# Kernel optimization log

Measured on AMD Instinct MI355X. Metric: run time of the kernel, lower is better.

Reference implementation:

```python
import jax, jax.numpy as jnp
import numpy as np

N_LAYERS = 2
ALPHA = 0.3
HAS_NORM = True
N_USERS = 100000
N_ITEMS = 50000
NNZ = 6400000
D = 64


def setup_inputs() -> dict:
    key = jax.random.key(0)
    ks = jax.random.split(key, 11)
    N = N_USERS + N_ITEMS
    return {
        "image_feats": jax.random.normal(ks[0], (N_ITEMS, 4096), dtype=jnp.float32),
        "text_feats": jax.random.normal(ks[1], (N_ITEMS, 384), dtype=jnp.float32),
        "image_pref": jax.random.normal(ks[2], (N_USERS, D), dtype=jnp.float32),
        "text_pref": jax.random.normal(ks[3], (N_USERS, D), dtype=jnp.float32),
        "W_img": jax.random.normal(ks[4], (4096, D), dtype=jnp.float32) * 0.02,
        "b_img": jax.random.normal(ks[5], (D,), dtype=jnp.float32) * 0.02,
        "W_txt": jax.random.normal(ks[6], (384, D), dtype=jnp.float32) * 0.02,
        "b_txt": jax.random.normal(ks[7], (D,), dtype=jnp.float32) * 0.02,
        "adj_vals": jax.random.uniform(ks[8], (NNZ,), dtype=jnp.float32),
        "adj_rows": jax.random.randint(ks[9], (NNZ,), 0, N, dtype=jnp.int32),
        "adj_cols": jax.random.randint(ks[10], (NNZ,), 0, N, dtype=jnp.int32),
    }


def _l2norm(x):
    # F.normalize(x, dim=1): x / max(||x||_2, eps)
    n = jnp.sqrt(jnp.sum(x * x, axis=1, keepdims=True))
    return x / jnp.maximum(n, 1e-12)


def reference(image_feats, text_feats, image_pref, text_pref,
              W_img, b_img, W_txt, b_txt, adj_vals, adj_rows, adj_cols):
    n_users = image_pref.shape[0]
    n_items = image_feats.shape[0]
    N = n_users + n_items

    image_emb = image_feats @ W_img + b_img  # [n_items, D]
    text_emb = text_feats @ W_txt + b_txt    # [n_items, D]
    if HAS_NORM:
        image_emb = _l2norm(image_emb)
        text_emb = _l2norm(text_emb)

    ego_i = jnp.concatenate([image_pref, image_emb], axis=0)  # [N, D]
    ego_t = jnp.concatenate([text_pref, text_emb], axis=0)    # [N, D]

    def spmm(x):
        # sparse COO matmul: out[r] += v * x[c]
        return jax.ops.segment_sum(adj_vals[:, None] * x[adj_cols], adj_rows,
                                   num_segments=N)

    for _ in range(N_LAYERS):
        ego_i = spmm(ego_i) + ALPHA * ego_i
        ego_t = spmm(ego_t) + ALPHA * ego_t

    user_pref = jnp.concatenate([ego_i[:n_users], ego_t[:n_users]], axis=1)
    items = jnp.concatenate([ego_i[n_users:], ego_t[n_users:]], axis=1)
    return user_pref, items
```

## Files before the change

### kernel.cpp

```cpp
#include <hip/hip_runtime.h>

#define N_USERS 100000
#define N_ITEMS 50000
#define NTOT    150000
#define DD      64
#define NNZV    6400000
#define ALPHA_  0.3f

#define BSHIFT  9
#define NBUCK   293
#define CH      16384
#define NCH     391

static constexpr size_t SZ = (size_t)NTOT * DD;

typedef unsigned int   u32;
typedef unsigned short u16;
typedef __attribute__((ext_vector_type(8))) short bf16x8;
typedef __attribute__((ext_vector_type(4))) float f32x4;

__device__ __forceinline__ u16 f2bf(float f) {
    u32 u = __float_as_uint(f);
    u += 0x7fffu + ((u >> 16) & 1u);
    return (u16)(u >> 16);
}
__device__ __forceinline__ float bf_lo(u32 w) { return __uint_as_float(w << 16); }
__device__ __forceinline__ float bf_hi(u32 w) { return __uint_as_float(w & 0xffff0000u); }

__global__ __launch_bounds__(256) void convert_wf(const float* __restrict__ W,
                                                  u32* __restrict__ Wf, int K)
{
    int tid = blockIdx.x * 256 + threadIdx.x;
    int total = (K >> 5) * 1024;
    if (tid >= total) return;
    int d  = tid & 3;
    int l  = (tid >> 2) & 63;
    int nt = (tid >> 8) & 3;
    int ks = tid >> 10;
    int k   = (ks << 5) + ((l >> 4) << 3) + (d << 1);
    int col = (nt << 4) + (l & 15);
    u16 lo = f2bf(W[(size_t)k * DD + col]);
    u16 hi = f2bf(W[(size_t)(k + 1) * DD + col]);
    Wf[tid] = (u32)lo | ((u32)hi << 16);
}

__global__ __launch_bounds__(256) void gemm_mfma(
    const float* __restrict__ A, const int4* __restrict__ Wf4,
    const float* __restrict__ bias, u16* __restrict__ bfp, int M, int K)
{
    const int w  = threadIdx.x >> 6;
    const int l  = threadIdx.x & 63;
    const int lr = l & 15;
    const int lk = l >> 4;
    const int rbase = blockIdx.x * 64 + w * 16;

    f32x4 acc0 = {0.f,0.f,0.f,0.f}, acc1 = acc0, acc2 = acc0, acc3 = acc0;

    int gr = rbase + lr; if (gr >= M) gr = M - 1;
    const float* ap = A + (size_t)gr * K + lk * 8;

    for (int ks = 0; ks < K; ks += 32) {
        float4 a0 = *(const float4*)(ap + ks);
        float4 a1 = *(const float4*)(ap + ks + 4);
        int4 av;
        av.x = (int)((u32)f2bf(a0.x) | ((u32)f2bf(a0.y) << 16));
        av.y = (int)((u32)f2bf(a0.z) | ((u32)f2bf(a0.w) << 16));
        av.z = (int)((u32)f2bf(a1.x) | ((u32)f2bf(a1.y) << 16));
        av.w = (int)((u32)f2bf(a1.z) | ((u32)f2bf(a1.w) << 16));
        bf16x8 af = *(bf16x8*)&av;
        const int4* wp = Wf4 + (size_t)(ks >> 5) * 256 + l;
        int4 w0 = wp[0], w1 = wp[64], w2 = wp[128], w3 = wp[192];
        acc0 = __builtin_amdgcn_mfma_f32_16x16x32_bf16(af, *(bf16x8*)&w0, acc0, 0, 0, 0);
        acc1 = __builtin_amdgcn_mfma_f32_16x16x32_bf16(af, *(bf16x8*)&w1, acc1, 0, 0, 0);
        acc2 = __builtin_amdgcn_mfma_f32_16x16x32_bf16(af, *(bf16x8*)&w2, acc2, 0, 0, 0);
        acc3 = __builtin_amdgcn_mfma_f32_16x16x32_bf16(af, *(bf16x8*)&w3, acc3, 0, 0, 0);
    }

    float bv0 = bias[lr], bv1 = bias[16 + lr], bv2 = bias[32 + lr], bv3 = bias[48 + lr];
    #pragma unroll
    for (int r = 0; r < 4; ++r) {
        float v0 = acc0[r] + bv0;
        float v1 = acc1[r] + bv1;
        float v2 = acc2[r] + bv2;
        float v3 = acc3[r] + bv3;
        float s = v0*v0 + v1*v1 + v2*v2 + v3*v3;
        s += __shfl_xor(s, 1); s += __shfl_xor(s, 2);
        s += __shfl_xor(s, 4); s += __shfl_xor(s, 8);
        float inv = 1.f / fmaxf(sqrtf(s), 1e-12f);
        int row = rbase + lk * 4 + r;
        if (row < M) {
            u16* bp = bfp + (size_t)row * 128;
            bp[lr]      = f2bf(v0 * inv);
            bp[16 + lr] = f2bf(v1 * inv);
            bp[32 + lr] = f2bf(v2 * inv);
            bp[48 + lr] = f2bf(v3 * inv);
        }
    }
}

__global__ __launch_bounds__(256) void build_user(const float4* __restrict__ ip,
                                                  const float4* __restrict__ tp,
                                                  ushort4* __restrict__ Xbf)
{
    int i = blockIdx.x * 256 + threadIdx.x;
    if (i >= N_USERS * 16) return;
    int row = i >> 4, q = i & 15;
    float4 vi = ip[i];
    float4 vt = tp[i];
    ushort4 bi; bi.x = f2bf(vi.x); bi.y = f2bf(vi.y); bi.z = f2bf(vi.z); bi.w = f2bf(vi.w);
    ushort4 bt; bt.x = f2bf(vt.x); bt.y = f2bf(vt.y); bt.z = f2bf(vt.z); bt.w = f2bf(vt.w);
    Xbf[(size_t)row * 32 + q]      = bi;
    Xbf[(size_t)row * 32 + 16 + q] = bt;
}

__global__ __launch_bounds__(256) void bucket_cnt(const int* __restrict__ rows,
                                                  int* __restrict__ gbhist)
{
    __shared__ int cnt[NBUCK];
    int t = threadIdx.x;
    for (int i = t; i < NBUCK; i += 256) cnt[i] = 0;
    __syncthreads();
    int beg = blockIdx.x * CH;
    int end = beg + CH; if (end > NNZV) end = NNZV;
    for (int i = beg + t; i < end; i += 256)
        atomicAdd(&cnt[rows[i] >> BSHIFT], 1);
    __syncthreads();
    for (int i = t; i < NBUCK; i += 256)
        if (cnt[i]) atomicAdd(&gbhist[i], cnt[i]);
}

__global__ __launch_bounds__(512) void scan_nbuck(const int* __restrict__ gbhist,
                                                  int* __restrict__ gbstart,
                                                  int* __restrict__ gbcur)
{
    __shared__ int sh[512];
    int t = threadIdx.x;
    int v = (t < NBUCK) ? gbhist[t] : 0;
    sh[t] = v;
    __syncthreads();
    for (int off = 1; off < 512; off <<= 1) {
        int x = (t >= off) ? sh[t - off] : 0;
        __syncthreads();
        sh[t] += x;
        __syncthreads();
    }
    if (t < NBUCK) {
        int e = sh[t] - v;
        gbstart[t] = e;
        gbcur[t]   = e;
    }
}

__global__ __launch_bounds__(256) void sort_pass1(
    const float* __restrict__ vals, const int* __restrict__ rows,
    const int* __restrict__ cols, int* __restrict__ gbcur,
    int2* __restrict__ ptmp)
{
    __shared__ int cnt[NBUCK];
    __shared__ int base[NBUCK];
    int t = threadIdx.x;
    int beg = blockIdx.x * CH;
    int end = beg + CH; if (end > NNZV) end = NNZV;

    for (int i = t; i < NBUCK; i += 256) cnt[i] = 0;
    __syncthreads();
    for (int i = beg + t; i < end; i += 256)
        atomicAdd(&cnt[rows[i] >> BSHIFT], 1);
    __syncthreads();
    for (int i = t; i < NBUCK; i += 256) {
        int c = cnt[i];
        base[i] = c ? atomicAdd(&gbcur[i], c) : 0;
    }
    __syncthreads();
    for (int i = t; i < NBUCK; i += 256) cnt[i] = 0;
    __syncthreads();
    for (int i = beg + t; i < end; i += 256) {
        int r = rows[i];
        int b = r >> BSHIFT;
        int rank = atomicAdd(&cnt[b], 1);
        int p = base[b] + rank;
        ptmp[p] = make_int2(__float_as_int(vals[i]), cols[i] | ((r & 511) << 18));
    }
}

__global__ __launch_bounds__(256) void sort_pass2(
    const int2* __restrict__ ptmp, const int* __restrict__ gbstart,
    int2* __restrict__ spair, int* __restrict__ rstart)
{
    __shared__ int rcnt[512];
    __shared__ int cur[512];
    __shared__ int s2[256];
    const int b = blockIdx.x;
    const int t = threadIdx.x;
    const int bstart = gbstart[b];
    const int bend   = (b == NBUCK - 1) ? NNZV : gbstart[b + 1];

    rcnt[t] = 0; rcnt[t + 256] = 0;
    __syncthreads();
    for (int i = bstart + t; i < bend; i += 256)
        atomicAdd(&rcnt[(ptmp[i].y >> 18) & 511], 1);
    __syncthreads();

    int a0 = rcnt[2 * t], a1 = rcnt[2 * t + 1];
    s2[t] = a0 + a1;
    __syncthreads();
    for (int off = 1; off < 256; off <<= 1) {
        int x = (t >= off) ? s2[t - off] : 0;
        __syncthreads();
        s2[t] += x;
        __syncthreads();
    }
    int epair = s2[t] - (a0 + a1);
    int c0 = bstart + epair;
    int c1 = c0 + a0;
    cur[2 * t]     = c0;
    cur[2 * t + 1] = c1;
    int r0 = (b << BSHIFT) + 2 * t;
    if (r0 < NTOT)     rstart[r0]     = c0;
    if (r0 + 1 < NTOT) rstart[r0 + 1] = c1;
    __syncthreads();

    for (int i = bstart + t; i < bend; i += 256) {
        int2 v = ptmp[i];
        int p = atomicAdd(&cur[(v.y >> 18) & 511], 1);
        spair[p] = make_int2(v.x, v.y & 0x3FFFF);
    }
}

__global__ void set_tail(int* __restrict__ rstart)
{
    if (threadIdx.x == 0 && blockIdx.x == 0) rstart[NTOT] = NNZV;
}

__global__ __launch_bounds__(256) void spmm_wave(
    const int2* __restrict__ spair, const int* __restrict__ rstart,
    const u32* __restrict__ Xbf, float* __restrict__ Xout,
    u32* __restrict__ XbfOut)
{
    int row = blockIdx.x * 4 + (threadIdx.x >> 6);
    int t   = threadIdx.x & 63;
    int beg = rstart[row];
    int end = rstart[row + 1];
    float a0 = 0.f, a1 = 0.f, b0 = 0.f, b1 = 0.f;
    int j = beg;
    for (; j + 8 <= end; j += 8) {
        int2 p0 = spair[j];     int2 p1 = spair[j + 1];
        int2 p2 = spair[j + 2]; int2 p3 = spair[j + 3];
        int2 p4 = spair[j + 4]; int2 p5 = spair[j + 5];
        int2 p6 = spair[j + 6]; int2 p7 = spair[j + 7];
        u32 w0 = Xbf[(size_t)p0.y * 64 + t];
        u32 w1 = Xbf[(size_t)p1.y * 64 + t];
        u32 w2 = Xbf[(size_t)p2.y * 64 + t];
        u32 w3 = Xbf[(size_t)p3.y * 64 + t];
        u32 w4 = Xbf[(size_t)p4.y * 64 + t];
        u32 w5 = Xbf[(size_t)p5.y * 64 + t];
        u32 w6 = Xbf[(size_t)p6.y * 64 + t];
        u32 w7 = Xbf[(size_t)p7.y * 64 + t];
        float v0 = __int_as_float(p0.x), v1 = __int_as_float(p1.x);
        float v2 = __int_as_float(p2.x), v3 = __int_as_float(p3.x);
        float v4 = __int_as_float(p4.x), v5 = __int_as_float(p5.x);
        float v6 = __int_as_float(p6.x), v7 = __int_as_float(p7.x);
        a0 += v0 * bf_lo(w0); a1 += v0 * bf_hi(w0);
        b0 += v1 * bf_lo(w1); b1 += v1 * bf_hi(w1);
        a0 += v2 * bf_lo(w2); a1 += v2 * bf_hi(w2);
        b0 += v3 * bf_lo(w3); b1 += v3 * bf_hi(w3);
        a0 += v4 * bf_lo(w4); a1 += v4 * bf_hi(w4);
        b0 += v5 * bf_lo(w5); b1 += v5 * bf_hi(w5);
        a0 += v6 * bf_lo(w6); a1 += v6 * bf_hi(w6);
        b0 += v7 * bf_lo(w7); b1 += v7 * bf_hi(w7);
    }
    for (; j < end; ++j) {
        int2 p = spair[j];
        u32 w = Xbf[(size_t)p.y * 64 + t];
        float v = __int_as_float(p.x);
        a0 += v * bf_lo(w); a1 += v * bf_hi(w);
    }
    u32 xr = Xbf[(size_t)row * 64 + t];
    float o0 = a0 + b0 + ALPHA_ * bf_lo(xr);
    float o1 = a1 + b1 + ALPHA_ * bf_hi(xr);
    if (Xout)
        *(float2*)(Xout + (size_t)row * 128 + 2 * t) = make_float2(o0, o1);
    if (XbfOut)
        XbfOut[(size_t)row * 64 + t] = (u32)f2bf(o0) | ((u32)f2bf(o1) << 16);
}

__global__ __launch_bounds__(256) void copy4(const float4* __restrict__ src,
                                             float4* __restrict__ dst, int n4)
{
    int i = blockIdx.x * 256 + threadIdx.x;
    if (i < n4) dst[i] = src[i];
}

__global__ __launch_bounds__(256) void gemm_bias(
    const float* __restrict__ A, const float* __restrict__ W,
    const float* __restrict__ bias, float* __restrict__ C, int M, int K, int ldc)
{
    __shared__ float As2[16][64];
    __shared__ float Bs2[16][64];
    const int t  = threadIdx.x;
    const int tx = t & 15, ty = t >> 4;
    const int lr = t >> 2;
    const int lk = (t & 3) << 2;
    const int brow = t >> 4;
    const int bc   = (t & 15) << 2;
    const int block_row = blockIdx.x << 6;

    float acc[4][4] = {{0.f,0.f,0.f,0.f},{0.f,0.f,0.f,0.f},{0.f,0.f,0.f,0.f},{0.f,0.f,0.f,0.f}};
    const int grow = block_row + lr;
    const bool arow_ok = (grow < M);
    const float* Aptr = A + (size_t)grow * K;

    for (int k0 = 0; k0 < K; k0 += 16) {
        float4 av = make_float4(0.f, 0.f, 0.f, 0.f);
        if (arow_ok) av = *(const float4*)(Aptr + k0 + lk);
        As2[lk+0][lr] = av.x; As2[lk+1][lr] = av.y; As2[lk+2][lr] = av.z; As2[lk+3][lr] = av.w;
        *(float4*)&Bs2[brow][bc] = *(const float4*)(W + (size_t)(k0 + brow) * DD + bc);
        __syncthreads();
        #pragma unroll
        for (int k = 0; k < 16; ++k) {
            float4 a = *(const float4*)&As2[k][ty << 2];
            float4 b = *(const float4*)&Bs2[k][tx << 2];
            acc[0][0] += a.x*b.x; acc[0][1] += a.x*b.y; acc[0][2] += a.x*b.z; acc[0][3] += a.x*b.w;
            acc[1][0] += a.y*b.x; acc[1][1] += a.y*b.y; acc[1][2] += a.y*b.z; acc[1][3] += a.y*b.w;
            acc[2][0] += a.z*b.x; acc[2][1] += a.z*b.y; acc[2][2] += a.z*b.z; acc[2][3] += a.z*b.w;
            acc[3][0] += a.w*b.x; acc[3][1] += a.w*b.y; acc[3][2] += a.w*b.z; acc[3][3] += a.w*b.w;
        }
        __syncthreads();
    }
    const float4 bv = *(const float4*)(bias + (tx << 2));
    #pragma unroll
    for (int i = 0; i < 4; ++i) {
        int row = block_row + (ty << 2) + i;
        if (row < M) {
            float4 o = make_float4(acc[i][0] + bv.x, acc[i][1] + bv.y,
                                   acc[i][2] + bv.z, acc[i][3] + bv.w);
            *(float4*)(C + (size_t)row * ldc + (tx << 2)) = o;
        }
    }
}

__global__ __launch_bounds__(256) void l2norm_rows(float* __restrict__ x, int nrows, int ld)
{
    int row  = blockIdx.x * 4 + (threadIdx.x >> 6);
    int lane = threadIdx.x & 63;
    if (row >= nrows) return;
    float v = x[(size_t)row * ld + lane];
    float s = v * v;
    #pragma unroll
    for (int off = 32; off > 0; off >>= 1) s += __shfl_xor(s, off);
    float n = sqrtf(s);
    x[(size_t)row * ld + lane] = v / fmaxf(n, 1e-12f);
}

__global__ __launch_bounds__(256) void scale4(const float4* __restrict__ src,
                                              float4* __restrict__ dst, int n4)
{
    int i = blockIdx.x * 256 + threadIdx.x;
    if (i < n4) {
        float4 v = src[i];
        dst[i] = make_float4(ALPHA_*v.x, ALPHA_*v.y, ALPHA_*v.z, ALPHA_*v.w);
    }
}

__global__ __launch_bounds__(256) void spmm_atomic(
    const float* __restrict__ vals, const int* __restrict__ rows,
    const int* __restrict__ cols, const float* __restrict__ x,
    float* __restrict__ out, int nnz)
{
    long long tid = (long long)blockIdx.x * 256 + threadIdx.x;
    int g = (int)(tid >> 4);
    if (g >= nnz) return;
    int lane = (int)(tid & 15);
    float v = vals[g];
    int r = rows[g], c = cols[g];
    float4 xv = *((const float4*)(x + (size_t)c * DD) + lane);
    float* o = out + (size_t)r * DD + (lane << 2);
    atomicAdd(o + 0, v * xv.x);
    atomicAdd(o + 1, v * xv.y);
    atomicAdd(o + 2, v * xv.z);
    atomicAdd(o + 3, v * xv.w);
}

__global__ __launch_bounds__(256) void finalize_k(
    const float4* __restrict__ egoI, const float4* __restrict__ egoT,
    float4* __restrict__ out)
{
    int tid = blockIdx.x * 256 + threadIdx.x;
    int row = tid >> 5, q = tid & 31;
    if (row >= NTOT) return;
    float4 v = (q < 16) ? egoI[(size_t)row * 16 + q] : egoT[(size_t)row * 16 + (q - 16)];
    out[tid] = v;
}

extern "C" void kernel_launch(void* const* d_in, const int* in_sizes, int n_in,
                              void* d_out, int out_size, void* d_ws, size_t ws_size,
                              hipStream_t stream)
{
    const float* image_feats = (const float*)d_in[0];
    const float* text_feats  = (const float*)d_in[1];
    const float* image_pref  = (const float*)d_in[2];
    const float* text_pref   = (const float*)d_in[3];
    const float* W_img       = (const float*)d_in[4];
    const float* b_img       = (const float*)d_in[5];
    const float* W_txt       = (const float*)d_in[6];
    const float* b_txt       = (const float*)d_in[7];
    const float* adj_vals    = (const float*)d_in[8];
    const int*   adj_rows    = (const int*)d_in[9];
    const int*   adj_cols    = (const int*)d_in[10];

    float* out = (float*)d_out;
    char*  ws  = (char*)d_ws;

    const size_t OFF_PTMP   = 0;
    const size_t OFF_SPAIR  = 51200000;
    const size_t OFF_RSTART = 102400000;
    const size_t OFF_SMALL  = 103000016;
    const size_t OFF_WFI    = 103004160;
    const size_t OFF_WFT    = 103528448;
    const size_t OFF_XB0    = 103577600;
    const size_t OFF_XB1    = 141977600;
    const size_t NEED       = 180377600;

    if (ws_size >= NEED) {
        int2* ptmp    = (int2*)(ws + OFF_PTMP);
        int2* spair   = (int2*)(ws + OFF_SPAIR);
        int*  rstart  = (int*) (ws + OFF_RSTART);
        int*  gbhist  = (int*) (ws + OFF_SMALL);
        int*  gbstart = gbhist + 320;
        int*  gbcur   = gbhist + 640;
        u32*  WfI     = (u32*) (ws + OFF_WFI);
        u32*  WfT     = (u32*) (ws + OFF_WFT);
        u32*  Xb0     = (u32*) (ws + OFF_XB0);
        u32*  Xb1     = (u32*) (ws + OFF_XB1);
        u16*  items_bf = (u16*)Xb0 + (size_t)N_USERS * 128;

        build_user<<<(N_USERS * 16) / 256, 256, 0, stream>>>(
            (const float4*)image_pref, (const float4*)text_pref, (ushort4*)Xb0);
        convert_wf<<<(4096 / 32 * 1024) / 256, 256, 0, stream>>>(W_img, WfI, 4096);
        convert_wf<<<(384 / 32 * 1024) / 256, 256, 0, stream>>>(W_txt, WfT, 384);

        hipMemsetAsync(gbhist, 0, 320 * sizeof(int), stream);
        bucket_cnt<<<NCH, 256, 0, stream>>>(adj_rows, gbhist);
        scan_nbuck<<<1, 512, 0, stream>>>(gbhist, gbstart, gbcur);
        sort_pass1<<<NCH, 256, 0, stream>>>(adj_vals, adj_rows, adj_cols, gbcur, ptmp);
        sort_pass2<<<NBUCK, 256, 0, stream>>>(ptmp, gbstart, spair, rstart);
        set_tail<<<1, 64, 0, stream>>>(rstart);

        gemm_mfma<<<(N_ITEMS + 63) / 64, 256, 0, stream>>>(
            image_feats, (const int4*)WfI, b_img, items_bf, N_ITEMS, 4096);
        gemm_mfma<<<(N_ITEMS + 63) / 64, 256, 0, stream>>>(
            text_feats, (const int4*)WfT, b_txt, items_bf + 64, N_ITEMS, 384);

        spmm_wave<<<NTOT / 4, 256, 0, stream>>>(spair, rstart, Xb0,
                                                (float*)nullptr, Xb1);
        spmm_wave<<<NTOT / 4, 256, 0, stream>>>(spair, rstart, Xb1,
                                                out, (u32*)nullptr);
        return;
    }

    float* wsf = (float*)d_ws;
    float* Ai = wsf;
    float* At = wsf + SZ;
    float* Bi = out;
    float* Bt = out + SZ;

    const int n4_pref = N_USERS * DD / 4;
    const int n4_ego  = (int)(SZ / 4);

    copy4<<<n4_pref / 256, 256, 0, stream>>>((const float4*)image_pref, (float4*)Ai, n4_pref);
    copy4<<<n4_pref / 256, 256, 0, stream>>>((const float4*)text_pref,  (float4*)At, n4_pref);

    gemm_bias<<<(N_ITEMS + 63) / 64, 256, 0, stream>>>(image_feats, W_img, b_img,
                                                       Ai + (size_t)N_USERS * DD, N_ITEMS, 4096, DD);
    gemm_bias<<<(N_ITEMS + 63) / 64, 256, 0, stream>>>(text_feats,  W_txt, b_txt,
                                                       At + (size_t)N_USERS * DD, N_ITEMS, 384, DD);
    l2norm_rows<<<(N_ITEMS + 3) / 4, 256, 0, stream>>>(Ai + (size_t)N_USERS * DD, N_ITEMS, DD);
    l2norm_rows<<<(N_ITEMS + 3) / 4, 256, 0, stream>>>(At + (size_t)N_USERS * DD, N_ITEMS, DD);

    const int spmm_blocks = (int)(((long long)NNZV * 16 + 255) / 256);

    scale4<<<(n4_ego + 255) / 256, 256, 0, stream>>>((const float4*)Ai, (float4*)Bi, n4_ego);
    spmm_atomic<<<spmm_blocks, 256, 0, stream>>>(adj_vals, adj_rows, adj_cols, Ai, Bi, NNZV);
    scale4<<<(n4_ego + 255) / 256, 256, 0, stream>>>((const float4*)At, (float4*)Bt, n4_ego);
    spmm_atomic<<<spmm_blocks, 256, 0, stream>>>(adj_vals, adj_rows, adj_cols, At, Bt, NNZV);

    scale4<<<(n4_ego + 255) / 256, 256, 0, stream>>>((const float4*)Bi, (float4*)Ai, n4_ego);
    spmm_atomic<<<spmm_blocks, 256, 0, stream>>>(adj_vals, adj_rows, adj_cols, Bi, Ai, NNZV);
    scale4<<<(n4_ego + 255) / 256, 256, 0, stream>>>((const float4*)Bt, (float4*)At, n4_ego);
    spmm_atomic<<<spmm_blocks, 256, 0, stream>>>(adj_vals, adj_rows, adj_cols, Bt, At, NNZV);

    finalize_k<<<(NTOT * 32) / 256, 256, 0, stream>>>((const float4*)Ai, (const float4*)At,
                                                      (float4*)out);
}
```

Before: 1.003 ms.

## Merge setup kernels, use finer buckets, prefetch GEMM loads, predicate SpMM tail

Folds user-embedding conversion and both weight conversions into one init kernel, and moves the rstart tail write into the scan kernel, cutting launch count. Halves the bucket width to 256 rows so the per-bucket row sort needs one counter per thread, and widens the counting and pass-1 blocks to 512 threads. The GEMM now loads the next A tile one step ahead to hide global-load latency. The SpMM inner loop drops its scalar remainder loop and instead handles the tail with clamped, predicated 8-wide loads, which adds wasted gathers on short rows.

```diff
diff --git a/kernel.cpp b/kernel.cpp
--- a/kernel.cpp
+++ b/kernel.cpp
@@ -7,8 +7,8 @@
 #define NNZV    6400000
 #define ALPHA_  0.3f
 
-#define BSHIFT  9
-#define NBUCK   293
+#define BSHIFT  8
+#define NBUCK   586
 #define CH      16384
 #define NCH     391
 
@@ -27,12 +27,9 @@
 __device__ __forceinline__ float bf_lo(u32 w) { return __uint_as_float(w << 16); }
 __device__ __forceinline__ float bf_hi(u32 w) { return __uint_as_float(w & 0xffff0000u); }
 
-__global__ __launch_bounds__(256) void convert_wf(const float* __restrict__ W,
-                                                  u32* __restrict__ Wf, int K)
-{
-    int tid = blockIdx.x * 256 + threadIdx.x;
-    int total = (K >> 5) * 1024;
-    if (tid >= total) return;
+__device__ __forceinline__ void convert_w_elem(const float* __restrict__ W,
+                                               u32* __restrict__ Wf, int tid)
+{
     int d  = tid & 3;
     int l  = (tid >> 2) & 63;
     int nt = (tid >> 8) & 3;
@@ -44,6 +41,31 @@
     Wf[tid] = (u32)lo | ((u32)hi << 16);
 }
 
+__global__ __launch_bounds__(256) void init_misc(
+    const float4* __restrict__ ip, const float4* __restrict__ tp,
+    ushort4* __restrict__ Xbf,
+    const float* __restrict__ Wi, u32* __restrict__ WfI,
+    const float* __restrict__ Wt, u32* __restrict__ WfT)
+{
+    int b = blockIdx.x;
+    if (b < 6250) {
+        int i = b * 256 + threadIdx.x;
+        int row = i >> 4, q = i & 15;
+        float4 vi = ip[i];
+        float4 vt = tp[i];
+        ushort4 bi; bi.x = f2bf(vi.x); bi.y = f2bf(vi.y); bi.z = f2bf(vi.z); bi.w = f2bf(vi.w);
+        ushort4 bt; bt.x = f2bf(vt.x); bt.y = f2bf(vt.y); bt.z = f2bf(vt.z); bt.w = f2bf(vt.w);
+        Xbf[(size_t)row * 32 + q]      = bi;
+        Xbf[(size_t)row * 32 + 16 + q] = bt;
+    } else if (b < 6250 + 512) {
+        int tid = (b - 6250) * 256 + threadIdx.x;
+        convert_w_elem(Wi, WfI, tid);
+    } else {
+        int tid = (b - 6762) * 256 + threadIdx.x;
+        convert_w_elem(Wt, WfT, tid);
+    }
+}
+
 __global__ __launch_bounds__(256) void gemm_mfma(
     const float* __restrict__ A, const int4* __restrict__ Wf4,
     const float* __restrict__ bias, u16* __restrict__ bfp, int M, int K)
@@ -59,14 +81,20 @@
     int gr = rbase + lr; if (gr >= M) gr = M - 1;
     const float* ap = A + (size_t)gr * K + lk * 8;
 
+    float4 ca0 = *(const float4*)(ap);
+    float4 ca1 = *(const float4*)(ap + 4);
+
     for (int ks = 0; ks < K; ks += 32) {
-        float4 a0 = *(const float4*)(ap + ks);
-        float4 a1 = *(const float4*)(ap + ks + 4);
+        float4 na0 = {0.f,0.f,0.f,0.f}, na1 = na0;
+        if (ks + 32 < K) {
+            na0 = *(const float4*)(ap + ks + 32);
+            na1 = *(const float4*)(ap + ks + 36);
+        }
         int4 av;
-        av.x = (int)((u32)f2bf(a0.x) | ((u32)f2bf(a0.y) << 16));
-        av.y = (int)((u32)f2bf(a0.z) | ((u32)f2bf(a0.w) << 16));
-        av.z = (int)((u32)f2bf(a1.x) | ((u32)f2bf(a1.y) << 16));
-        av.w = (int)((u32)f2bf(a1.z) | ((u32)f2bf(a1.w) << 16));
+        av.x = (int)((u32)f2bf(ca0.x) | ((u32)f2bf(ca0.y) << 16));
+        av.y = (int)((u32)f2bf(ca0.z) | ((u32)f2bf(ca0.w) << 16));
+        av.z = (int)((u32)f2bf(ca1.x) | ((u32)f2bf(ca1.y) << 16));
+        av.w = (int)((u32)f2bf(ca1.z) | ((u32)f2bf(ca1.w) << 16));
         bf16x8 af = *(bf16x8*)&av;
         const int4* wp = Wf4 + (size_t)(ks >> 5) * 256 + l;
         int4 w0 = wp[0], w1 = wp[64], w2 = wp[128], w3 = wp[192];
@@ -74,6 +102,7 @@
         acc1 = __builtin_amdgcn_mfma_f32_16x16x32_bf16(af, *(bf16x8*)&w1, acc1, 0, 0, 0);
         acc2 = __builtin_amdgcn_mfma_f32_16x16x32_bf16(af, *(bf16x8*)&w2, acc2, 0, 0, 0);
         acc3 = __builtin_amdgcn_mfma_f32_16x16x32_bf16(af, *(bf16x8*)&w3, acc3, 0, 0, 0);
+        ca0 = na0; ca1 = na1;
     }
 
     float bv0 = bias[lr], bv1 = bias[16 + lr], bv2 = bias[32 + lr], bv3 = bias[48 + lr];
@@ -98,47 +127,33 @@
     }
 }
 
-__global__ __launch_bounds__(256) void build_user(const float4* __restrict__ ip,
-                                                  const float4* __restrict__ tp,
-                                                  ushort4* __restrict__ Xbf)
-{
-    int i = blockIdx.x * 256 + threadIdx.x;
-    if (i >= N_USERS * 16) return;
-    int row = i >> 4, q = i & 15;
-    float4 vi = ip[i];
-    float4 vt = tp[i];
-    ushort4 bi; bi.x = f2bf(vi.x); bi.y = f2bf(vi.y); bi.z = f2bf(vi.z); bi.w = f2bf(vi.w);
-    ushort4 bt; bt.x = f2bf(vt.x); bt.y = f2bf(vt.y); bt.z = f2bf(vt.z); bt.w = f2bf(vt.w);
-    Xbf[(size_t)row * 32 + q]      = bi;
-    Xbf[(size_t)row * 32 + 16 + q] = bt;
-}
-
-__global__ __launch_bounds__(256) void bucket_cnt(const int* __restrict__ rows,
+__global__ __launch_bounds__(512) void bucket_cnt(const int* __restrict__ rows,
                                                   int* __restrict__ gbhist)
 {
     __shared__ int cnt[NBUCK];
     int t = threadIdx.x;
-    for (int i = t; i < NBUCK; i += 256) cnt[i] = 0;
+    for (int i = t; i < NBUCK; i += 512) cnt[i] = 0;
     __syncthreads();
     int beg = blockIdx.x * CH;
     int end = beg + CH; if (end > NNZV) end = NNZV;
-    for (int i = beg + t; i < end; i += 256)
+    for (int i = beg + t; i < end; i += 512)
         atomicAdd(&cnt[rows[i] >> BSHIFT], 1);
     __syncthreads();
-    for (int i = t; i < NBUCK; i += 256)
+    for (int i = t; i < NBUCK; i += 512)
         if (cnt[i]) atomicAdd(&gbhist[i], cnt[i]);
 }
 
-__global__ __launch_bounds__(512) void scan_nbuck(const int* __restrict__ gbhist,
-                                                  int* __restrict__ gbstart,
-                                                  int* __restrict__ gbcur)
-{
-    __shared__ int sh[512];
+__global__ __launch_bounds__(1024) void scan_nbuck(const int* __restrict__ gbhist,
+                                                   int* __restrict__ gbstart,
+                                                   int* __restrict__ gbcur,
+                                                   int* __restrict__ rstart)
+{
+    __shared__ int sh[1024];
     int t = threadIdx.x;
     int v = (t < NBUCK) ? gbhist[t] : 0;
     sh[t] = v;
     __syncthreads();
-    for (int off = 1; off < 512; off <<= 1) {
+    for (int off = 1; off < 1024; off <<= 1) {
         int x = (t >= off) ? sh[t - off] : 0;
         __syncthreads();
         sh[t] += x;
@@ -149,9 +164,10 @@
         gbstart[t] = e;
         gbcur[t]   = e;
     }
-}
-
-__global__ __launch_bounds__(256) void sort_pass1(
+    if (t == 0) rstart[NTOT] = NNZV;
+}
+
+__global__ __launch_bounds__(512) void sort_pass1(
     const float* __restrict__ vals, const int* __restrict__ rows,
     const int* __restrict__ cols, int* __restrict__ gbcur,
     int2* __restrict__ ptmp)
@@ -162,24 +178,24 @@
     int beg = blockIdx.x * CH;
     int end = beg + CH; if (end > NNZV) end = NNZV;
 
-    for (int i = t; i < NBUCK; i += 256) cnt[i] = 0;
-    __syncthreads();
-    for (int i = beg + t; i < end; i += 256)
+    for (int i = t; i < NBUCK; i += 512) cnt[i] = 0;
+    __syncthreads();
+    for (int i = beg + t; i < end; i += 512)
         atomicAdd(&cnt[rows[i] >> BSHIFT], 1);
     __syncthreads();
-    for (int i = t; i < NBUCK; i += 256) {
+    for (int i = t; i < NBUCK; i += 512) {
         int c = cnt[i];
         base[i] = c ? atomicAdd(&gbcur[i], c) : 0;
     }
     __syncthreads();
-    for (int i = t; i < NBUCK; i += 256) cnt[i] = 0;
-    __syncthreads();
-    for (int i = beg + t; i < end; i += 256) {
+    for (int i = t; i < NBUCK; i += 512) cnt[i] = 0;
+    __syncthreads();
+    for (int i = beg + t; i < end; i += 512) {
         int r = rows[i];
         int b = r >> BSHIFT;
         int rank = atomicAdd(&cnt[b], 1);
         int p = base[b] + rank;
-        ptmp[p] = make_int2(__float_as_int(vals[i]), cols[i] | ((r & 511) << 18));
+        ptmp[p] = make_int2(__float_as_int(vals[i]), cols[i] | ((r & 255) << 18));
     }
 }
 
@@ -187,49 +203,40 @@
     const int2* __restrict__ ptmp, const int* __restrict__ gbstart,
     int2* __restrict__ spair, int* __restrict__ rstart)
 {
-    __shared__ int rcnt[512];
-    __shared__ int cur[512];
-    __shared__ int s2[256];
+    __shared__ int rcnt[256];
+    __shared__ int sh[256];
+    __shared__ int cur[256];
     const int b = blockIdx.x;
     const int t = threadIdx.x;
     const int bstart = gbstart[b];
     const int bend   = (b == NBUCK - 1) ? NNZV : gbstart[b + 1];
 
-    rcnt[t] = 0; rcnt[t + 256] = 0;
+    rcnt[t] = 0;
     __syncthreads();
     for (int i = bstart + t; i < bend; i += 256)
-        atomicAdd(&rcnt[(ptmp[i].y >> 18) & 511], 1);
-    __syncthreads();
-
-    int a0 = rcnt[2 * t], a1 = rcnt[2 * t + 1];
-    s2[t] = a0 + a1;
+        atomicAdd(&rcnt[(ptmp[i].y >> 18) & 255], 1);
+    __syncthreads();
+
+    int v = rcnt[t];
+    sh[t] = v;
     __syncthreads();
     for (int off = 1; off < 256; off <<= 1) {
-        int x = (t >= off) ? s2[t - off] : 0;
-        __syncthreads();
-        s2[t] += x;
-        __syncthreads();
-    }
-    int epair = s2[t] - (a0 + a1);
-    int c0 = bstart + epair;
-    int c1 = c0 + a0;
-    cur[2 * t]     = c0;
-    cur[2 * t + 1] = c1;
-    int r0 = (b << BSHIFT) + 2 * t;
-    if (r0 < NTOT)     rstart[r0]     = c0;
-    if (r0 + 1 < NTOT) rstart[r0 + 1] = c1;
+        int x = (t >= off) ? sh[t - off] : 0;
+        __syncthreads();
+        sh[t] += x;
+        __syncthreads();
+    }
+    int c = bstart + sh[t] - v;
+    cur[t] = c;
+    int r0 = (b << BSHIFT) + t;
+    if (r0 < NTOT) rstart[r0] = c;
     __syncthreads();
 
     for (int i = bstart + t; i < bend; i += 256) {
-        int2 v = ptmp[i];
-        int p = atomicAdd(&cur[(v.y >> 18) & 511], 1);
-        spair[p] = make_int2(v.x, v.y & 0x3FFFF);
-    }
-}
-
-__global__ void set_tail(int* __restrict__ rstart)
-{
-    if (threadIdx.x == 0 && blockIdx.x == 0) rstart[NTOT] = NNZV;
+        int2 pv = ptmp[i];
+        int p = atomicAdd(&cur[(pv.y >> 18) & 255], 1);
+        spair[p] = make_int2(pv.x, pv.y & 0x3FFFF);
+    }
 }
 
 __global__ __launch_bounds__(256) void spmm_wave(
@@ -242,38 +249,23 @@
     int beg = rstart[row];
     int end = rstart[row + 1];
     float a0 = 0.f, a1 = 0.f, b0 = 0.f, b1 = 0.f;
-    int j = beg;
-    for (; j + 8 <= end; j += 8) {
-        int2 p0 = spair[j];     int2 p1 = spair[j + 1];
-        int2 p2 = spair[j + 2]; int2 p3 = spair[j + 3];
-        int2 p4 = spair[j + 4]; int2 p5 = spair[j + 5];
-        int2 p6 = spair[j + 6]; int2 p7 = spair[j + 7];
-        u32 w0 = Xbf[(size_t)p0.y * 64 + t];
-        u32 w1 = Xbf[(size_t)p1.y * 64 + t];
-        u32 w2 = Xbf[(size_t)p2.y * 64 + t];
-        u32 w3 = Xbf[(size_t)p3.y * 64 + t];
-        u32 w4 = Xbf[(size_t)p4.y * 64 + t];
-        u32 w5 = Xbf[(size_t)p5.y * 64 + t];
-        u32 w6 = Xbf[(size_t)p6.y * 64 + t];
-        u32 w7 = Xbf[(size_t)p7.y * 64 + t];
-        float v0 = __int_as_float(p0.x), v1 = __int_as_float(p1.x);
-        float v2 = __int_as_float(p2.x), v3 = __int_as_float(p3.x);
-        float v4 = __int_as_float(p4.x), v5 = __int_as_float(p5.x);
-        float v6 = __int_as_float(p6.x), v7 = __int_as_float(p7.x);
-        a0 += v0 * bf_lo(w0); a1 += v0 * bf_hi(w0);
-        b0 += v1 * bf_lo(w1); b1 += v1 * bf_hi(w1);
-        a0 += v2 * bf_lo(w2); a1 += v2 * bf_hi(w2);
-        b0 += v3 * bf_lo(w3); b1 += v3 * bf_hi(w3);
-        a0 += v4 * bf_lo(w4); a1 += v4 * bf_hi(w4);
-        b0 += v5 * bf_lo(w5); b1 += v5 * bf_hi(w5);
-        a0 += v6 * bf_lo(w6); a1 += v6 * bf_hi(w6);
-        b0 += v7 * bf_lo(w7); b1 += v7 * bf_hi(w7);
-    }
-    for (; j < end; ++j) {
-        int2 p = spair[j];
-        u32 w = Xbf[(size_t)p.y * 64 + t];
-        float v = __int_as_float(p.x);
-        a0 += v * bf_lo(w); a1 += v * bf_hi(w);
+    for (int j = beg; j < end; j += 8) {
+        int2 p[8];
+        #pragma unroll
+        for (int s = 0; s < 8; ++s) {
+            int idx = j + s;
+            p[s] = spair[idx < end ? idx : end - 1];
+        }
+        u32 wv[8];
+        #pragma unroll
+        for (int s = 0; s < 8; ++s)
+            wv[s] = Xbf[(size_t)p[s].y * 64 + t];
+        #pragma unroll
+        for (int s = 0; s < 8; ++s) {
+            float v = (j + s < end) ? __int_as_float(p[s].x) : 0.f;
+            if (s & 1) { b0 += v * bf_lo(wv[s]); b1 += v * bf_hi(wv[s]); }
+            else       { a0 += v * bf_lo(wv[s]); a1 += v * bf_hi(wv[s]); }
+        }
     }
     u32 xr = Xbf[(size_t)row * 64 + t];
     float o0 = a0 + b0 + ALPHA_ * bf_lo(xr);
@@ -414,37 +406,35 @@
     const size_t OFF_PTMP   = 0;
     const size_t OFF_SPAIR  = 51200000;
     const size_t OFF_RSTART = 102400000;
-    const size_t OFF_SMALL  = 103000016;
-    const size_t OFF_WFI    = 103004160;
-    const size_t OFF_WFT    = 103528448;
-    const size_t OFF_XB0    = 103577600;
-    const size_t OFF_XB1    = 141977600;
-    const size_t NEED       = 180377600;
+    const size_t OFF_SMALL  = 103000064;
+    const size_t OFF_WFI    = 103007744;
+    const size_t OFF_WFT    = 103532032;
+    const size_t OFF_XB0    = 103581184;
+    const size_t OFF_XB1    = 141981184;
+    const size_t NEED       = 180381184;
 
     if (ws_size >= NEED) {
         int2* ptmp    = (int2*)(ws + OFF_PTMP);
         int2* spair   = (int2*)(ws + OFF_SPAIR);
         int*  rstart  = (int*) (ws + OFF_RSTART);
         int*  gbhist  = (int*) (ws + OFF_SMALL);
-        int*  gbstart = gbhist + 320;
-        int*  gbcur   = gbhist + 640;
+        int*  gbstart = gbhist + 640;
+        int*  gbcur   = gbhist + 1280;
         u32*  WfI     = (u32*) (ws + OFF_WFI);
         u32*  WfT     = (u32*) (ws + OFF_WFT);
         u32*  Xb0     = (u32*) (ws + OFF_XB0);
         u32*  Xb1     = (u32*) (ws + OFF_XB1);
         u16*  items_bf = (u16*)Xb0 + (size_t)N_USERS * 128;
 
-        build_user<<<(N_USERS * 16) / 256, 256, 0, stream>>>(
-            (const float4*)image_pref, (const float4*)text_pref, (ushort4*)Xb0);
-        convert_wf<<<(4096 / 32 * 1024) / 256, 256, 0, stream>>>(W_img, WfI, 4096);
-        convert_wf<<<(384 / 32 * 1024) / 256, 256, 0, stream>>>(W_txt, WfT, 384);
-
-        hipMemsetAsync(gbhist, 0, 320 * sizeof(int), stream);
-        bucket_cnt<<<NCH, 256, 0, stream>>>(adj_rows, gbhist);
-        scan_nbuck<<<1, 512, 0, stream>>>(gbhist, gbstart, gbcur);
-        sort_pass1<<<NCH, 256, 0, stream>>>(adj_vals, adj_rows, adj_cols, gbcur, ptmp);
+        init_misc<<<6810, 256, 0, stream>>>(
+            (const float4*)image_pref, (const float4*)text_pref, (ushort4*)Xb0,
+            W_img, WfI, W_txt, WfT);
+
+        hipMemsetAsync(gbhist, 0, 640 * sizeof(int), stream);
+        bucket_cnt<<<NCH, 512, 0, stream>>>(adj_rows, gbhist);
+        scan_nbuck<<<1, 1024, 0, stream>>>(gbhist, gbstart, gbcur, rstart);
+        sort_pass1<<<NCH, 512, 0, stream>>>(adj_vals, adj_rows, adj_cols, gbcur, ptmp);
         sort_pass2<<<NBUCK, 256, 0, stream>>>(ptmp, gbstart, spair, rstart);
-        set_tail<<<1, 64, 0, stream>>>(rstart);
 
         gemm_mfma<<<(N_ITEMS + 63) / 64, 256, 0, stream>>>(
             image_feats, (const int4*)WfI, b_img, items_bf, N_ITEMS, 4096);
```

Result: slower. 1.026 ms (+2.2%).
